# Kernel tuning notes

Hardware: AMD Instinct MI355X
Metric: run time of the kernel (lower is better)

## Reference

```python
import jax, jax.numpy as jnp
import numpy as np

N = 50000      # nodes
E = 1600000    # edges (before self-loops)
IN = 128       # in_chnl
H = 2          # heads
C = 64         # out_chnl per head
NEG_SLOPE = 0.2


def setup_inputs() -> dict:
    key = jax.random.key(0)
    k1, k2, k3, k4, k5 = jax.random.split(key, 5)
    h_node = jax.random.normal(k1, (N, IN), dtype=jnp.float32)
    edge_index = jax.random.randint(k2, (2, E), 0, N, dtype=jnp.int32)
    s = 1.0 / np.sqrt(IN)
    W = (jax.random.normal(k3, (IN, H * C), dtype=jnp.float32) * s)
    att_src = jax.random.normal(k4, (H, C), dtype=jnp.float32) * s
    att_dst = jax.random.normal(k5, (H, C), dtype=jnp.float32) * s
    bias = jnp.zeros((H * C,), dtype=jnp.float32)
    return {"h_node": h_node, "edge_index": edge_index, "W": W,
            "att_src": att_src, "att_dst": att_dst, "bias": bias}


def reference(h_node, edge_index, W, att_src, att_dst, bias):
    # dropout is identity in eval mode
    src, dst = edge_index[0], edge_index[1]
    # PyG GATConv default: add self-loops
    loops = jnp.arange(N, dtype=src.dtype)
    src = jnp.concatenate([src, loops])
    dst = jnp.concatenate([dst, loops])

    x = (h_node @ W).reshape(N, H, C)              # [N,H,C] projected features
    a_s = jnp.sum(x * att_src, axis=-1)            # [N,H] source attention terms
    a_d = jnp.sum(x * att_dst, axis=-1)            # [N,H] dest attention terms

    e = jax.nn.leaky_relu(a_s[src] + a_d[dst], NEG_SLOPE)        # [E+N,H]
    # segment softmax over edges grouped by destination node
    m = jax.lax.stop_gradient(jax.ops.segment_max(e, dst, num_segments=N))
    ex = jnp.exp(e - m[dst])
    den = jax.ops.segment_sum(ex, dst, num_segments=N)           # [N,H]
    alpha = ex / den[dst]                                        # [E+N,H]

    out = jax.ops.segment_sum(alpha[:, :, None] * x[src], dst, num_segments=N)
    out = out.reshape(N, H * C) + bias             # concat=True -> [N, H*C]
    return jax.nn.elu(out)
```

## Files before the change

### kernel.cpp

```cpp
#include <hip/hip_runtime.h>
#include <hip/hip_bf16.h>

#define NN 50000
#define EE 1600000
#define TOT (EE + NN)
#define INC 128
#define HC 128
#define NEG_SLOPE 0.2f

#define EPB 4096
#define NB1 ((TOT + EPB - 1) / EPB)
#define RNG 128
#define NR ((NN + RNG - 1) / RNG)
#define CAPR 4864
#define NPB 4
#define MAXD 136
#define PROJB ((NN + 63) / 64)

__device__ __forceinline__ unsigned short f2bf(float f) {
    __hip_bfloat16 b = __float2bfloat16(f);
    return *reinterpret_cast<unsigned short*>(&b);
}

#define LOADW(dst, kk)                                                        \
    _Pragma("unroll") for (int q = 0; q < 4; q++) {                           \
        float4 wv4 = *reinterpret_cast<const float4*>(&W[(size_t)((kk) + q) * HC + j2 * 4]); \
        dst[q][0] = wv4.x; dst[q][1] = wv4.y; dst[q][2] = wv4.z; dst[q][3] = wv4.w; \
    }

#define FMAS(wv, kk)                                                          \
    _Pragma("unroll") for (int r8 = 0; r8 < 8; r8++) {                        \
        const float* hr = hs + (rg * 8 + r8) * INC + (kk);                    \
        float4 hv = *reinterpret_cast<const float4*>(hr);                     \
        _Pragma("unroll") for (int c = 0; c < 4; c++)                         \
            acc[r8][c] += hv.x * wv[0][c] + hv.y * wv[1][c]                   \
                        + hv.z * wv[2][c] + hv.w * wv[3][c];                  \
    }

__device__ __forceinline__ void proj_body(
        char* smem, int pb,
        const float* __restrict__ h, const float* __restrict__ W,
        const float* __restrict__ att_src, const float* __restrict__ att_dst,
        __hip_bfloat16* __restrict__ x_bf,
        float* __restrict__ a_s, float* __restrict__ a_d) {
    float* hs = (float*)smem;
    const int t = threadIdx.x;
    const int row0 = pb * 64;

    for (int q = t; q < 64 * 32; q += 256) {
        int rr = q >> 5;
        int c4 = (q & 31) << 2;
        int gr = row0 + rr;
        float4 v = (gr < NN) ? *reinterpret_cast<const float4*>(&h[(size_t)gr * INC + c4])
                             : make_float4(0.f, 0.f, 0.f, 0.f);
        *reinterpret_cast<float4*>(&hs[rr * INC + c4]) = v;
    }
    __syncthreads();

    const int j2 = t & 31;
    const int rg = t >> 5;
    float acc[8][4];
#pragma unroll
    for (int r8 = 0; r8 < 8; r8++)
#pragma unroll
        for (int c = 0; c < 4; c++) acc[r8][c] = 0.f;

    float wA[4][4], wB[4][4];
    LOADW(wA, 0)
    for (int k = 0; k < INC; k += 8) {
        LOADW(wB, k + 4)
        FMAS(wA, k)
        if (k + 8 < INC) { LOADW(wA, k + 8) }
        FMAS(wB, k + 4)
    }

#pragma unroll
    for (int r8 = 0; r8 < 8; r8++) {
        int gr = row0 + rg * 8 + r8;
        if (gr < NN) {
            ushort4 sv;
            sv.x = f2bf(acc[r8][0]);
            sv.y = f2bf(acc[r8][1]);
            sv.z = f2bf(acc[r8][2]);
            sv.w = f2bf(acc[r8][3]);
            *reinterpret_cast<ushort4*>(&x_bf[(size_t)gr * HC + j2 * 4]) = sv;
        }
    }

    const int lane = t & 63;
    const int hidx = j2 >> 4;
    const float4 avs = *reinterpret_cast<const float4*>(&att_src[j2 * 4]);
    const float4 avd = *reinterpret_cast<const float4*>(&att_dst[j2 * 4]);
#pragma unroll
    for (int r8 = 0; r8 < 8; r8++) {
        float ps = acc[r8][0] * avs.x + acc[r8][1] * avs.y
                 + acc[r8][2] * avs.z + acc[r8][3] * avs.w;
        float pd = acc[r8][0] * avd.x + acc[r8][1] * avd.y
                 + acc[r8][2] * avd.z + acc[r8][3] * avd.w;
#pragma unroll
        for (int o = 1; o < 16; o <<= 1) {
            ps += __shfl_xor(ps, o);
            pd += __shfl_xor(pd, o);
        }
        int gr = row0 + rg * 8 + r8;
        if ((lane & 15) == 0 && gr < NN) {
            a_s[gr * 2 + hidx] = ps;
            a_d[gr * 2 + hidx] = pd;
        }
    }
}

__device__ __forceinline__ void bin_body(
        char* smem, int b,
        const int* __restrict__ ei,
        unsigned int* __restrict__ gbin, unsigned short* __restrict__ bofs) {
    int* cnt = (int*)smem;
    int* ofs = cnt + NR;
    int* cur = ofs + NR + 1;
    int* wsum = cur + NR;
    unsigned int* lbuf = (unsigned int*)(wsum + 4);
    const int t = threadIdx.x;

    for (int i = t; i < NR; i += 256) cnt[i] = 0;
    __syncthreads();

    unsigned int pk[16];
    bool vd[16];
#pragma unroll
    for (int q = 0; q < 16; q++) {
        int i = b * EPB + q * 256 + t;
        vd[q] = (i < TOT);
        int s, d;
        if (i < EE)       { s = ei[i]; d = ei[EE + i]; }
        else if (i < TOT) { s = d = i - EE; }
        else              { s = d = 0; }
        pk[q] = ((unsigned int)(d >> 7) << 23) |
                ((unsigned int)(d & 127) << 16) | (unsigned int)s;
        if (vd[q]) atomicAdd(&cnt[pk[q] >> 23], 1);
    }
    __syncthreads();

    {
        int v0 = (2 * t < NR) ? cnt[2 * t] : 0;
        int v1 = (2 * t + 1 < NR) ? cnt[2 * t + 1] : 0;
        int ps = v0 + v1;
        int sc = ps;
        int lane = t & 63, wid = t >> 6;
#pragma unroll
        for (int o = 1; o < 64; o <<= 1) {
            int u = __shfl_up(sc, o);
            if (lane >= o) sc += u;
        }
        if (lane == 63) wsum[wid] = sc;
        __syncthreads();
        int woff = 0;
        for (int ww = 0; ww < wid; ww++) woff += wsum[ww];
        int excl = woff + sc - ps;
        if (2 * t <= NR) ofs[2 * t] = excl;
        if (2 * t < NR) cur[2 * t] = excl;
        if (2 * t + 1 <= NR) ofs[2 * t + 1] = excl + v0;
        if (2 * t + 1 < NR) cur[2 * t + 1] = excl + v0;
    }
    __syncthreads();

#pragma unroll
    for (int q = 0; q < 16; q++) {
        if (vd[q]) {
            int pos = atomicAdd(&cur[pk[q] >> 23], 1);
            lbuf[pos] = pk[q];
        }
    }
    __syncthreads();

#pragma unroll
    for (int q = 0; q < 16; q++)
        gbin[(size_t)b * EPB + q * 256 + t] = lbuf[q * 256 + t];
    for (int i = t; i <= NR; i += 256)
        bofs[(size_t)b * (NR + 1) + i] = (unsigned short)ofs[i];
}

__global__ __launch_bounds__(256) void gat_fused1(
        const float* __restrict__ h, const float* __restrict__ W,
        const float* __restrict__ att_src, const float* __restrict__ att_dst,
        const int* __restrict__ ei,
        unsigned int* __restrict__ gbin, unsigned short* __restrict__ bofs,
        __hip_bfloat16* __restrict__ x_bf,
        float* __restrict__ a_s, float* __restrict__ a_d) {
    __shared__ __align__(16) char smem[64 * INC * 4];
    if (blockIdx.x < NB1)
        bin_body(smem, blockIdx.x, ei, gbin, bofs);
    else
        proj_body(smem, blockIdx.x - NB1, h, W, att_src, att_dst, x_bf, a_s, a_d);
}

__global__ __launch_bounds__(256) void gat_build(const unsigned int* __restrict__ gbin,
                                                 const unsigned short* __restrict__ bofs,
                                                 unsigned short* __restrict__ csr,
                                                 int* __restrict__ start32,
                                                 int* __restrict__ deg32) {
    __shared__ unsigned int est[CAPR];
    __shared__ int deg[RNG];
    __shared__ int ofs[RNG + 1];
    __shared__ int cur[RNG];
    __shared__ int wsum[4];
    __shared__ int etot;
    const int t = threadIdx.x;
    const int r = blockIdx.x;

    for (int i = t; i < CAPR; i += 256) est[i] = 0xFFFFFFFFu;
    for (int i = t; i < RNG; i += 256) { deg[i] = 0; cur[i] = 0; }
    if (t == 0) etot = 0;
    __syncthreads();

    for (int sb = t; sb < NB1; sb += 256) {
        int o0 = (int)bofs[(size_t)sb * (NR + 1) + r];
        int o1 = (int)bofs[(size_t)sb * (NR + 1) + r + 1];
        int c = o1 - o0;
        if (c <= 0) continue;
        int ao = atomicAdd(&etot, c);
        if (ao + c > CAPR) continue;
        const unsigned int* src = gbin + (size_t)sb * EPB + o0;
        for (int q = 0; q < c; q++) est[ao + q] = src[q];
    }
    __syncthreads();

    const int tot = min(etot, CAPR);
    for (int i = t; i < tot; i += 256) {
        unsigned int e = est[i];
        if (e != 0xFFFFFFFFu) atomicAdd(&deg[(e >> 16) & 127], 1);
    }
    __syncthreads();

    {
        int v = (t < RNG) ? deg[t] : 0;
        int sc = v;
        int lane = t & 63, wid = t >> 6;
#pragma unroll
        for (int o = 1; o < 64; o <<= 1) {
            int u = __shfl_up(sc, o);
            if (lane >= o) sc += u;
        }
        if (lane == 63) wsum[wid] = sc;
        __syncthreads();
        int woff = 0;
        for (int ww = 0; ww < wid; ww++) woff += wsum[ww];
        int excl = woff + sc - v;
        if (t < RNG) ofs[t] = excl;
        if (t == RNG - 1) ofs[RNG] = excl + v;
    }
    __syncthreads();

    const int rbase = r * CAPR;
    for (int i = t; i < tot; i += 256) {
        unsigned int e = est[i];
        if (e == 0xFFFFFFFFu) continue;
        int dl = (e >> 16) & 127;
        int pos = atomicAdd(&cur[dl], 1);
        csr[(size_t)rbase + ofs[dl] + pos] = (unsigned short)(e & 0xFFFFu);
    }
    __syncthreads();

    if (t < RNG) {
        int n = r * RNG + t;
        if (n < NN) {
            start32[n] = rbase + ofs[t];
            deg32[n] = deg[t];
        }
    }
}

__global__ __launch_bounds__(256) void gat_aggr(
        const uint4* __restrict__ x16,
        const float2* __restrict__ a_s2, const float2* __restrict__ a_d2,
        const int* __restrict__ start32, const int* __restrict__ deg32,
        const unsigned short* __restrict__ csr,
        const float4* __restrict__ bias4, float4* __restrict__ out4) {
    __shared__ int    s_src[NPB][MAXD];
    __shared__ float2 s_p[NPB][MAXD];
    const int w    = threadIdx.x >> 6;
    const int lane = threadIdx.x & 63;
    const int n    = blockIdx.x * NPB + w;
    if (n >= NN) return;

    const int deg  = min(deg32[n], MAXD - 4);
    const int base = start32[n];
    const float2 ad = a_d2[n];

    float d0 = 0.f, d1 = 0.f;
    for (int jj = lane; jj < deg; jj += 64) {
        int s = (int)csr[(size_t)base + jj];
        s_src[w][jj] = s;
        float2 as = a_s2[s];
        float e0 = as.x + ad.x; e0 = (e0 > 0.f) ? e0 : NEG_SLOPE * e0;
        float e1 = as.y + ad.y; e1 = (e1 > 0.f) ? e1 : NEG_SLOPE * e1;
        float p0 = __expf(e0), p1 = __expf(e1);
        s_p[w][jj] = make_float2(p0, p1);
        d0 += p0;
        d1 += p1;
    }
    if (lane < 4) {
        s_src[w][deg + lane] = 0;
        s_p[w][deg + lane] = make_float2(0.f, 0.f);
    }
#pragma unroll
    for (int off = 32; off; off >>= 1) {
        d0 += __shfl_xor(d0, off);
        d1 += __shfl_xor(d1, off);
    }

    const int sub = lane >> 4;
    const int cl  = lane & 15;
    const int hd  = cl >> 3;
    const float* __restrict__ pwl = &s_p[w][0].x + hd;

    float a0=0.f,a1=0.f,a2=0.f,a3=0.f,a4=0.f,a5=0.f,a6=0.f,a7=0.f;
    const int ng = (deg + 3) >> 2;
    int g = 0;
    for (; g + 4 <= ng; g += 4) {
#pragma unroll
        for (int k = 0; k < 4; k++) {
            int e = 4 * (g + k) + sub;
            int s = s_src[w][e];
            uint4 u = x16[(size_t)s * 16 + cl];
            float wk = pwl[2 * e];
            a0 += wk * __uint_as_float(u.x << 16);
            a1 += wk * __uint_as_float(u.x & 0xffff0000u);
            a2 += wk * __uint_as_float(u.y << 16);
            a3 += wk * __uint_as_float(u.y & 0xffff0000u);
            a4 += wk * __uint_as_float(u.z << 16);
            a5 += wk * __uint_as_float(u.z & 0xffff0000u);
            a6 += wk * __uint_as_float(u.w << 16);
            a7 += wk * __uint_as_float(u.w & 0xffff0000u);
        }
    }
    for (; g < ng; g++) {
        int e = 4 * g + sub;
        int s = s_src[w][e];
        uint4 u = x16[(size_t)s * 16 + cl];
        float wk = pwl[2 * e];
        a0 += wk * __uint_as_float(u.x << 16);
        a1 += wk * __uint_as_float(u.x & 0xffff0000u);
        a2 += wk * __uint_as_float(u.y << 16);
        a3 += wk * __uint_as_float(u.y & 0xffff0000u);
        a4 += wk * __uint_as_float(u.z << 16);
        a5 += wk * __uint_as_float(u.z & 0xffff0000u);
        a6 += wk * __uint_as_float(u.w << 16);
        a7 += wk * __uint_as_float(u.w & 0xffff0000u);
    }
#define MRG(a) a += __shfl_xor(a, 16); a += __shfl_xor(a, 32);
    MRG(a0) MRG(a1) MRG(a2) MRG(a3) MRG(a4) MRG(a5) MRG(a6) MRG(a7)
#undef MRG

    if (lane < 16) {
        const float invd = 1.0f / (hd ? d1 : d0);
        float4 b0 = bias4[cl * 2];
        float4 b1 = bias4[cl * 2 + 1];
        float4 o0, o1;
        o0.x = a0 * invd + b0.x;  o0.y = a1 * invd + b0.y;
        o0.z = a2 * invd + b0.z;  o0.w = a3 * invd + b0.w;
        o1.x = a4 * invd + b1.x;  o1.y = a5 * invd + b1.y;
        o1.z = a6 * invd + b1.z;  o1.w = a7 * invd + b1.w;
        o0.x = (o0.x > 0.f) ? o0.x : expm1f(o0.x);
        o0.y = (o0.y > 0.f) ? o0.y : expm1f(o0.y);
        o0.z = (o0.z > 0.f) ? o0.z : expm1f(o0.z);
        o0.w = (o0.w > 0.f) ? o0.w : expm1f(o0.w);
        o1.x = (o1.x > 0.f) ? o1.x : expm1f(o1.x);
        o1.y = (o1.y > 0.f) ? o1.y : expm1f(o1.y);
        o1.z = (o1.z > 0.f) ? o1.z : expm1f(o1.z);
        o1.w = (o1.w > 0.f) ? o1.w : expm1f(o1.w);
        out4[(size_t)n * 32 + cl * 2] = o0;
        out4[(size_t)n * 32 + cl * 2 + 1] = o1;
    }
}

static inline size_t align256(size_t v) { return (v + 255) & ~(size_t)255; }

extern "C" void kernel_launch(void* const* d_in, const int* in_sizes, int n_in,
                              void* d_out, int out_size, void* d_ws, size_t ws_size,
                              hipStream_t stream) {
    const float* h_node  = (const float*)d_in[0];
    const int*   ei      = (const int*)d_in[1];
    const float* W       = (const float*)d_in[2];
    const float* att_src = (const float*)d_in[3];
    const float* att_dst = (const float*)d_in[4];
    const float* bias    = (const float*)d_in[5];
    float* out = (float*)d_out;

    char* base = (char*)d_ws;
    size_t off = 0;
    __hip_bfloat16* x_bf = (__hip_bfloat16*)(base + off);
    off = align256(off + (size_t)NN * HC * 2);
    float* a_s = (float*)(base + off);      off = align256(off + (size_t)NN * 2 * 4);
    float* a_d = (float*)(base + off);      off = align256(off + (size_t)NN * 2 * 4);
    unsigned int* gbin = (unsigned int*)(base + off);
    off = align256(off + (size_t)NB1 * EPB * 4);
    unsigned short* bofs = (unsigned short*)(base + off);
    off = align256(off + (size_t)NB1 * (NR + 1) * 2);
    unsigned short* csr = (unsigned short*)(base + off);
    off = align256(off + (size_t)NR * CAPR * 2);
    int* start32 = (int*)(base + off);      off = align256(off + (size_t)NN * 4);
    int* deg32 = (int*)(base + off);        off = align256(off + (size_t)NN * 4);
    (void)ws_size;

    gat_fused1<<<NB1 + PROJB, 256, 0, stream>>>(h_node, W, att_src, att_dst, ei,
                                                gbin, bofs, x_bf, a_s, a_d);
    gat_build<<<NR, 256, 0, stream>>>(gbin, bofs, csr, start32, deg32);
    gat_aggr<<<(NN + NPB - 1) / NPB, 256, 0, stream>>>((const uint4*)x_bf,
                                                       (const float2*)a_s,
                                                       (const float2*)a_d,
                                                       start32, deg32, csr,
                                                       (const float4*)bias,
                                                       (float4*)out);
}
```

Measured before the change: 198.9 us.

## Pair projection with CSR build instead of binning in fused launch

Moves the node projection blocks out of the binning launch and into the CSR-build launch. Binning now runs alone in a kernel with a smaller shared-memory footprint, and the build and projection blocks share one grid. The build kernel is a small grid (NR blocks) that would otherwise leave the GPU underused. Its shared arrays are carved from the 32KB projection buffer, and the build blocks are scheduled first. The binning kernel's shared-memory size is now set explicitly, and it may now get higher occupancy.

```diff
diff --git a/kernel.cpp b/kernel.cpp
--- a/kernel.cpp
+++ b/kernel.cpp
@@ -179,37 +179,23 @@
         bofs[(size_t)b * (NR + 1) + i] = (unsigned short)ofs[i];
 }
 
-__global__ __launch_bounds__(256) void gat_fused1(
-        const float* __restrict__ h, const float* __restrict__ W,
-        const float* __restrict__ att_src, const float* __restrict__ att_dst,
-        const int* __restrict__ ei,
-        unsigned int* __restrict__ gbin, unsigned short* __restrict__ bofs,
-        __hip_bfloat16* __restrict__ x_bf,
-        float* __restrict__ a_s, float* __restrict__ a_d) {
-    __shared__ __align__(16) char smem[64 * INC * 4];
-    if (blockIdx.x < NB1)
-        bin_body(smem, blockIdx.x, ei, gbin, bofs);
-    else
-        proj_body(smem, blockIdx.x - NB1, h, W, att_src, att_dst, x_bf, a_s, a_d);
-}
-
-__global__ __launch_bounds__(256) void gat_build(const unsigned int* __restrict__ gbin,
-                                                 const unsigned short* __restrict__ bofs,
-                                                 unsigned short* __restrict__ csr,
-                                                 int* __restrict__ start32,
-                                                 int* __restrict__ deg32) {
-    __shared__ unsigned int est[CAPR];
-    __shared__ int deg[RNG];
-    __shared__ int ofs[RNG + 1];
-    __shared__ int cur[RNG];
-    __shared__ int wsum[4];
-    __shared__ int etot;
+__device__ __forceinline__ void build_body(
+        char* smem, int r,
+        const unsigned int* __restrict__ gbin,
+        const unsigned short* __restrict__ bofs,
+        unsigned short* __restrict__ csr,
+        int* __restrict__ start32, int* __restrict__ deg32) {
+    unsigned int* est = (unsigned int*)smem;
+    int* deg  = (int*)(est + CAPR);
+    int* ofs  = deg + RNG;
+    int* cur  = ofs + RNG + 1;
+    int* wsum = cur + RNG;
+    int* etot = wsum + 4;
     const int t = threadIdx.x;
-    const int r = blockIdx.x;
 
     for (int i = t; i < CAPR; i += 256) est[i] = 0xFFFFFFFFu;
     for (int i = t; i < RNG; i += 256) { deg[i] = 0; cur[i] = 0; }
-    if (t == 0) etot = 0;
+    if (t == 0) *etot = 0;
     __syncthreads();
 
     for (int sb = t; sb < NB1; sb += 256) {
@@ -217,14 +203,14 @@
         int o1 = (int)bofs[(size_t)sb * (NR + 1) + r + 1];
         int c = o1 - o0;
         if (c <= 0) continue;
-        int ao = atomicAdd(&etot, c);
+        int ao = atomicAdd(etot, c);
         if (ao + c > CAPR) continue;
         const unsigned int* src = gbin + (size_t)sb * EPB + o0;
         for (int q = 0; q < c; q++) est[ao + q] = src[q];
     }
     __syncthreads();
 
-    const int tot = min(etot, CAPR);
+    const int tot = min(*etot, CAPR);
     for (int i = t; i < tot; i += 256) {
         unsigned int e = est[i];
         if (e != 0xFFFFFFFFu) atomicAdd(&deg[(e >> 16) & 127], 1);
@@ -267,6 +253,28 @@
             deg32[n] = deg[t];
         }
     }
+}
+
+__global__ __launch_bounds__(256) void gat_bin(
+        const int* __restrict__ ei,
+        unsigned int* __restrict__ gbin, unsigned short* __restrict__ bofs) {
+    __shared__ __align__(16) char smem[(3 * NR + 5) * 4 + EPB * 4];
+    bin_body(smem, blockIdx.x, ei, gbin, bofs);
+}
+
+__global__ __launch_bounds__(256) void gat_fused2(
+        const float* __restrict__ h, const float* __restrict__ W,
+        const float* __restrict__ att_src, const float* __restrict__ att_dst,
+        const unsigned int* __restrict__ gbin, const unsigned short* __restrict__ bofs,
+        unsigned short* __restrict__ csr,
+        int* __restrict__ start32, int* __restrict__ deg32,
+        __hip_bfloat16* __restrict__ x_bf,
+        float* __restrict__ a_s, float* __restrict__ a_d) {
+    __shared__ __align__(16) char smem[64 * INC * 4];
+    if (blockIdx.x < NR)
+        build_body(smem, blockIdx.x, gbin, bofs, csr, start32, deg32);
+    else
+        proj_body(smem, blockIdx.x - NR, h, W, att_src, att_dst, x_bf, a_s, a_d);
 }
 
 __global__ __launch_bounds__(256) void gat_aggr(
@@ -402,9 +410,10 @@
     int* deg32 = (int*)(base + off);        off = align256(off + (size_t)NN * 4);
     (void)ws_size;
 
-    gat_fused1<<<NB1 + PROJB, 256, 0, stream>>>(h_node, W, att_src, att_dst, ei,
-                                                gbin, bofs, x_bf, a_s, a_d);
-    gat_build<<<NR, 256, 0, stream>>>(gbin, bofs, csr, start32, deg32);
+    gat_bin<<<NB1, 256, 0, stream>>>(ei, gbin, bofs);
+    gat_fused2<<<NR + PROJB, 256, 0, stream>>>(h_node, W, att_src, att_dst,
+                                               gbin, bofs, csr, start32, deg32,
+                                               x_bf, a_s, a_d);
     gat_aggr<<<(NN + NPB - 1) / NPB, 256, 0, stream>>>((const uint4*)x_bf,
                                                        (const float2*)a_s,
                                                        (const float2*)a_d,
```

Result: no change. 195.6 us (-1.6%).

## Gather bin segments with prefix scan and per-edge binary search in CSR build

Applied to the files above, without the earlier changes.

Replaces the per-thread serial copy of each source block's bin segment (with an atomic slot allocation) by a block-wide prefix scan over segment counts. Each thread then fetches individual edges, locating its segment by binary search, so global reads are coalesced and load-balanced. The degree count is folded into the same pass, and the block grows to 512 threads. The sentinel fill and its checks are dropped. This adds a log-depth search per edge and requires NB1 <= 512 so one scan covers all segments.

```diff
diff --git a/kernel.cpp b/kernel.cpp
--- a/kernel.cpp
+++ b/kernel.cpp
@@ -193,72 +193,89 @@
         proj_body(smem, blockIdx.x - NB1, h, W, att_src, att_dst, x_bf, a_s, a_d);
 }
 
-__global__ __launch_bounds__(256) void gat_build(const unsigned int* __restrict__ gbin,
-                                                 const unsigned short* __restrict__ bofs,
-                                                 unsigned short* __restrict__ csr,
-                                                 int* __restrict__ start32,
-                                                 int* __restrict__ deg32) {
+__global__ __launch_bounds__(512) void gat_build2(
+        const unsigned int* __restrict__ gbin,
+        const unsigned short* __restrict__ bofs,
+        unsigned short* __restrict__ csr,
+        int* __restrict__ start32,
+        int* __restrict__ deg32) {
     __shared__ unsigned int est[CAPR];
+    __shared__ int sbase[512];
+    __shared__ int segofs[NB1];
     __shared__ int deg[RNG];
     __shared__ int ofs[RNG + 1];
     __shared__ int cur[RNG];
-    __shared__ int wsum[4];
-    __shared__ int etot;
+    __shared__ int wsum[8];
+    __shared__ int tot_sh;
     const int t = threadIdx.x;
     const int r = blockIdx.x;
-
-    for (int i = t; i < CAPR; i += 256) est[i] = 0xFFFFFFFFu;
-    for (int i = t; i < RNG; i += 256) { deg[i] = 0; cur[i] = 0; }
-    if (t == 0) etot = 0;
-    __syncthreads();
-
-    for (int sb = t; sb < NB1; sb += 256) {
-        int o0 = (int)bofs[(size_t)sb * (NR + 1) + r];
-        int o1 = (int)bofs[(size_t)sb * (NR + 1) + r + 1];
-        int c = o1 - o0;
-        if (c <= 0) continue;
-        int ao = atomicAdd(&etot, c);
-        if (ao + c > CAPR) continue;
-        const unsigned int* src = gbin + (size_t)sb * EPB + o0;
-        for (int q = 0; q < c; q++) est[ao + q] = src[q];
-    }
-    __syncthreads();
-
-    const int tot = min(etot, CAPR);
-    for (int i = t; i < tot; i += 256) {
-        unsigned int e = est[i];
-        if (e != 0xFFFFFFFFu) atomicAdd(&deg[(e >> 16) & 127], 1);
+    const int lane = t & 63, wid = t >> 6;
+
+    int c = 0;
+    if (t < NB1) {
+        int o0 = (int)bofs[(size_t)t * (NR + 1) + r];
+        int o1 = (int)bofs[(size_t)t * (NR + 1) + r + 1];
+        c = o1 - o0;
+        segofs[t] = o0;
+    }
+    int sc = c;
+#pragma unroll
+    for (int o = 1; o < 64; o <<= 1) {
+        int u = __shfl_up(sc, o);
+        if (lane >= o) sc += u;
+    }
+    if (lane == 63) wsum[wid] = sc;
+    if (t < RNG) { deg[t] = 0; cur[t] = 0; }
+    __syncthreads();
+    int woff = 0;
+    for (int ww = 0; ww < wid; ww++) woff += wsum[ww];
+    int excl = woff + sc - c;
+    sbase[t] = excl;
+    if (t == 511) tot_sh = excl + c;
+    __syncthreads();
+
+    const int tot = min(tot_sh, CAPR);
+
+    for (int e = t; e < tot; e += 512) {
+        int lo = 0, hi = NB1 - 1;
+        while (lo < hi) {
+            int mid = (lo + hi + 1) >> 1;
+            if (sbase[mid] <= e) lo = mid; else hi = mid - 1;
+        }
+        unsigned int v = gbin[(size_t)lo * EPB + segofs[lo] + (e - sbase[lo])];
+        est[e] = v;
+        atomicAdd(&deg[(v >> 16) & 127], 1);
     }
     __syncthreads();
 
     {
         int v = (t < RNG) ? deg[t] : 0;
-        int sc = v;
-        int lane = t & 63, wid = t >> 6;
-#pragma unroll
-        for (int o = 1; o < 64; o <<= 1) {
-            int u = __shfl_up(sc, o);
-            if (lane >= o) sc += u;
-        }
-        if (lane == 63) wsum[wid] = sc;
-        __syncthreads();
-        int woff = 0;
-        for (int ww = 0; ww < wid; ww++) woff += wsum[ww];
-        int excl = woff + sc - v;
-        if (t < RNG) ofs[t] = excl;
-        if (t == RNG - 1) ofs[RNG] = excl + v;
+        if (t < 128) {
+            int sc2 = v;
+#pragma unroll
+            for (int o = 1; o < 64; o <<= 1) {
+                int u = __shfl_up(sc2, o);
+                if (lane >= o) sc2 += u;
+            }
+            if (lane == 63) wsum[wid] = sc2;
+            __syncthreads();
+            int woff2 = (wid == 1) ? wsum[0] : 0;
+            int excl2 = woff2 + sc2 - v;
+            ofs[t] = excl2;
+            if (t == 127) ofs[RNG] = excl2 + v;
+        } else {
+            __syncthreads();
+        }
     }
     __syncthreads();
 
     const int rbase = r * CAPR;
-    for (int i = t; i < tot; i += 256) {
+    for (int i = t; i < tot; i += 512) {
         unsigned int e = est[i];
-        if (e == 0xFFFFFFFFu) continue;
         int dl = (e >> 16) & 127;
         int pos = atomicAdd(&cur[dl], 1);
         csr[(size_t)rbase + ofs[dl] + pos] = (unsigned short)(e & 0xFFFFu);
     }
-    __syncthreads();
 
     if (t < RNG) {
         int n = r * RNG + t;
@@ -404,7 +421,7 @@
 
     gat_fused1<<<NB1 + PROJB, 256, 0, stream>>>(h_node, W, att_src, att_dst, ei,
                                                 gbin, bofs, x_bf, a_s, a_d);
-    gat_build<<<NR, 256, 0, stream>>>(gbin, bofs, csr, start32, deg32);
+    gat_build2<<<NR, 512, 0, stream>>>(gbin, bofs, csr, start32, deg32);
     gat_aggr<<<(NN + NPB - 1) / NPB, 256, 0, stream>>>((const uint4*)x_bf,
                                                        (const float2*)a_s,
                                                        (const float2*)a_d,
```

After: 194.7 us. 1.02x faster.
